# Optimization experiments

Hardware: AMD Instinct MI355X
Metric: run time of the kernel (lower is better)

Reference implementation:

```python
import jax, jax.numpy as jnp
import numpy as np

B, C, N = 8, 128, 4096
C2 = C // 2
BN_EPS = 1e-5


def setup_inputs() -> dict:
    key = jax.random.key(0)
    ks = jax.random.split(key, 8)
    s = 1.0 / np.sqrt(C)
    s2 = 1.0 / np.sqrt(C2)
    return {
        "x": jax.random.normal(ks[0], (B, C, N), dtype=jnp.float32),
        "w_qk": jax.random.uniform(ks[1], (C2, C), jnp.float32, -s, s),  # shared q/k weight
        "w_v": jax.random.uniform(ks[2], (C2, C), jnp.float32, -s, s),
        "b_v": jax.random.uniform(ks[3], (C2,), jnp.float32, -s, s),
        "w_x": jax.random.uniform(ks[4], (C2, C), jnp.float32, -s, s),
        "w_t": jax.random.uniform(ks[5], (C2, C2), jnp.float32, -s2, s2),
        "b_t": jax.random.uniform(ks[6], (C2,), jnp.float32, -s2, s2),
        "gamma": jnp.ones((C2,), jnp.float32),
        "beta": jnp.zeros((C2,), jnp.float32),
    }


def reference(x, w_qk, w_v, b_v, w_x, w_t, b_t, gamma, beta):
    # 1x1 convs are per-point linear maps: [B,C,N] -> [B,C2,N]
    x_q = jnp.einsum("oc,bcn->bno", w_qk, x)          # [B, N, C2]
    x_k = jnp.einsum("oc,bcn->bon", w_qk, x)          # [B, C2, N]
    x_v = jnp.einsum("oc,bcn->bon", w_v, x) + b_v[None, :, None]

    energy = jnp.einsum("bno,bom->bnm", x_q, x_k)     # [B, N, N]
    attn = jax.nn.softmax(energy, axis=-1)            # row softmax
    attn = attn / (1e-9 + attn.sum(axis=1, keepdims=True))  # column L1 renorm

    x_r = jnp.einsum("bon,bnm->bom", x_v, attn)       # [B, C2, N]
    x_c = jnp.einsum("oc,bcn->bon", w_x, x)           # [B, C2, N]

    d = x_c - x_r
    t = jnp.einsum("oi,bin->bon", w_t, d) + b_t[None, :, None]
    # BatchNorm1d (training-mode batch stats) over (B, N) per channel
    mean = t.mean(axis=(0, 2), keepdims=True)
    var = t.var(axis=(0, 2), keepdims=True)
    t_hat = (t - mean) * jax.lax.rsqrt(var + BN_EPS)
    x_r2 = jax.nn.relu(gamma[None, :, None] * t_hat + beta[None, :, None])
    return x_c + x_r2
```

## Files before the change

kernel.cpp:

```cpp
#include <hip/hip_runtime.h>

#define B_   8
#define C_   128
#define N_   4096
#define C2_  64

typedef __bf16 bf16x8 __attribute__((ext_vector_type(8)));
typedef float  f32x4  __attribute__((ext_vector_type(4)));

#define MFMA16(a, b, c) __builtin_amdgcn_mfma_f32_16x16x32_bf16((a), (b), (c), 0, 0, 0)

#define QK_SCALE 1.2011224087864498f

static __device__ __forceinline__ unsigned short f2bf(float f) {
    union { __bf16 b; unsigned short u; } cv;
    cv.b = (__bf16)f;
    return cv.u;
}

struct us4 { unsigned short a, b, c, d; };

static __device__ __forceinline__ void gl_lds16(const unsigned short* g, void* l) {
    __builtin_amdgcn_global_load_lds(
        (const __attribute__((address_space(1))) unsigned int*)g,
        (__attribute__((address_space(3))) unsigned int*)l,
        16, 0, 0);
}

__global__ __launch_bounds__(256) void k1_proj(
    const float* __restrict__ x, const float* __restrict__ w_qk,
    const float* __restrict__ w_v, const float* __restrict__ b_v,
    const float* __restrict__ w_x,
    unsigned short* __restrict__ qk_t, unsigned short* __restrict__ xv_bf,
    float* __restrict__ xc)
{
    __shared__ __align__(16) unsigned short w_lds[192 * 136];
    __shared__ __align__(16) unsigned short x_t[64 * 136];
    const int tid = threadIdx.x;
    const int wave = tid >> 6, lane = tid & 63;
    const int quad = lane >> 4, col = lane & 15;
    const int b = blockIdx.y;
    const int n0 = blockIdx.x * 64;

    const float* wsrc[3] = {w_qk, w_v, w_x};
    #pragma unroll
    for (int mat = 0; mat < 3; ++mat) {
        const float* wm = wsrc[mat];
        #pragma unroll
        for (int it = 0; it < 8; ++it) {
            const int idx = it * 256 + tid;
            const int o = idx >> 5, c = (idx & 31) * 4;
            const float4 v = *(const float4*)(wm + o * C_ + c);
            us4 pk;
            pk.a = f2bf(v.x); pk.b = f2bf(v.y); pk.c = f2bf(v.z); pk.d = f2bf(v.w);
            *(us4*)&w_lds[(mat * 64 + o) * 136 + c] = pk;
        }
    }
    const float* xb = x + (size_t)b * C_ * N_ + n0;
    #pragma unroll
    for (int it = 0; it < 8; ++it) {
        const int idx = it * 256 + tid;
        const int c = idx >> 4, n = (idx & 15) * 4;
        const float4 v = *(const float4*)(xb + (size_t)c * N_ + n);
        x_t[(n + 0) * 136 + c] = f2bf(v.x);
        x_t[(n + 1) * 136 + c] = f2bf(v.y);
        x_t[(n + 2) * 136 + c] = f2bf(v.z);
        x_t[(n + 3) * 136 + c] = f2bf(v.w);
    }
    __syncthreads();

    const int nw = wave * 16;
    bf16x8 bfr[4];
    #pragma unroll
    for (int kt = 0; kt < 4; ++kt)
        bfr[kt] = *(const bf16x8*)&x_t[(nw + col) * 136 + kt * 32 + quad * 8];

    const int n_g = n0 + nw + col;

    #pragma unroll
    for (int ot = 0; ot < 12; ++ot) {
        f32x4 acc = {0.f, 0.f, 0.f, 0.f};
        #pragma unroll
        for (int kt = 0; kt < 4; ++kt) {
            const bf16x8 afr = *(const bf16x8*)&w_lds[(ot * 16 + col) * 136 + kt * 32 + quad * 8];
            acc = MFMA16(afr, bfr[kt], acc);
        }
        if (ot < 4) {
            us4 pk;
            pk.a = f2bf(acc[0] * QK_SCALE); pk.b = f2bf(acc[1] * QK_SCALE);
            pk.c = f2bf(acc[2] * QK_SCALE); pk.d = f2bf(acc[3] * QK_SCALE);
            *(us4*)&qk_t[(size_t)(b * N_ + n_g) * C2_ + ot * 16 + quad * 4] = pk;
        } else if (ot < 8) {
            const float4 bv4 = *(const float4*)(b_v + (ot - 4) * 16 + quad * 4);
            const float* bvp = (const float*)&bv4;
            #pragma unroll
            for (int r = 0; r < 4; ++r)
                xv_bf[(size_t)(b * C2_ + (ot - 4) * 16 + quad * 4 + r) * N_ + n_g]
                    = f2bf(acc[r] + bvp[r]);
        } else {
            #pragma unroll
            for (int r = 0; r < 4; ++r)
                xc[(size_t)(b * C2_ + (ot - 8) * 16 + quad * 4 + r) * N_ + n_g] = acc[r];
        }
    }
}

__global__ __launch_bounds__(256) void k2_rowstats(
    const unsigned short* __restrict__ qk_t, float* __restrict__ part_rs)
{
    __shared__ __align__(16) unsigned char lds_raw[2 * 8192];
    const int tid = threadIdx.x;
    const int wave = tid >> 6, lane = tid & 63;
    const int quad = lane >> 4, col = lane & 15;
    const int b = blockIdx.x & 7;
    const int nblk = (blockIdx.x >> 3) & 31;
    const int mq = blockIdx.x >> 8;
    const int n_base = nblk * 128 + wave * 32;
    const int m_start = mq * 1024;
    const unsigned short* qb = qk_t + (size_t)b * N_ * C2_;

    bf16x8 a0[2], a1[2];
    #pragma unroll
    for (int s = 0; s < 2; ++s) {
        const unsigned short* p = qb + (size_t)(n_base + s * 16 + col) * C2_ + quad * 8;
        a0[s] = *(const bf16x8*)p;
        a1[s] = *(const bf16x8*)(p + 32);
    }

    auto stage = [&](int m0, int p) {
        unsigned char* base = lds_raw + p * 8192;
        #pragma unroll
        for (int r = 0; r < 2; ++r) {
            const int idx = r * 256 + tid;
            const int row = idx >> 3, seg = idx & 7;
            gl_lds16(qb + (size_t)(m0 + row) * C2_ + (size_t)(seg ^ (row & 7)) * 8,
                     base + idx * 16);
        }
    };

    float run_s[2][4] = {{0.f, 0.f, 0.f, 0.f}, {0.f, 0.f, 0.f, 0.f}};
    stage(m_start, 0);
    __syncthreads();

    for (int c = 0; c < 16; ++c) {
        const int p = c & 1;
        if (c + 1 < 16) stage(m_start + (c + 1) * 64, 1 - p);
        const unsigned short* qt = (const unsigned short*)(lds_raw + p * 8192);
        #pragma unroll
        for (int ms = 0; ms < 4; ++ms) {
            const int row = ms * 16 + col;
            const bf16x8 b0 = *(const bf16x8*)(qt + row * 64 + ((quad ^ (col & 7)) * 8));
            const bf16x8 b1 = *(const bf16x8*)(qt + row * 64 + (((4 + quad) ^ (col & 7)) * 8));
            #pragma unroll
            for (int s = 0; s < 2; ++s) {
                f32x4 acc = {0.f, 0.f, 0.f, 0.f};
                acc = MFMA16(a0[s], b0, acc);
                acc = MFMA16(a1[s], b1, acc);
                #pragma unroll
                for (int r = 0; r < 4; ++r)
                    run_s[s][r] += __builtin_amdgcn_exp2f(acc[r]);
            }
        }
        __syncthreads();
    }

    #pragma unroll
    for (int s = 0; s < 2; ++s)
        #pragma unroll
        for (int r = 0; r < 4; ++r) {
            #pragma unroll
            for (int off = 1; off < 16; off <<= 1)
                run_s[s][r] += __shfl_xor(run_s[s][r], off, 64);
        }
    if (col == 0) {
        #pragma unroll
        for (int s = 0; s < 2; ++s)
            #pragma unroll
            for (int r = 0; r < 4; ++r)
                part_rs[((size_t)(mq * 8 + b) << 12) + n_base + s * 16 + quad * 4 + r]
                    = run_s[s][r];
    }
}

__global__ __launch_bounds__(256) void k2b_comb(
    const float* __restrict__ part_rs, float* __restrict__ rowoff)
{
    const int i = blockIdx.x * 256 + threadIdx.x;
    const int b = i >> 12, n = i & 4095;
    float s = 0.f;
    #pragma unroll
    for (int q = 0; q < 4; ++q)
        s += part_rs[((size_t)(q * 8 + b) << 12) + n];
    rowoff[i] = __builtin_amdgcn_logf(s);
}

__global__ __launch_bounds__(256) void k3_pv(
    const unsigned short* __restrict__ qk_t, const unsigned short* __restrict__ xv_bf,
    const float* __restrict__ rowoff, float* __restrict__ yp0, float* __restrict__ yp1,
    float* __restrict__ yp2, float* __restrict__ cspart)
{
    __shared__ __align__(16) unsigned char lds_raw[32768 + 8 * 2304];
    const int tid = threadIdx.x;
    const int wave = tid >> 6, lane = tid & 63;
    const int quad = lane >> 4, col = lane & 15;
    const int b = blockIdx.x & 7;
    const int m_blk = ((blockIdx.x >> 3) & 31) * 128;
    const int sk = blockIdx.x >> 8;
    const int n_start = (sk == 0) ? 0 : 1408 + (sk - 1) * 1344;
    const int n_chunks = (sk == 0) ? 22 : 21;
    const int m_wave = m_blk + wave * 32;
    const unsigned short* qb = qk_t + (size_t)b * N_ * C2_;
    const unsigned short* vb = xv_bf + (size_t)b * C2_ * N_;
    const float* ro = rowoff + b * N_;
    float* yp = (sk == 0) ? yp0 : (sk == 1) ? yp1 : yp2;

    bf16x8 kb0[2], kb1[2];
    #pragma unroll
    for (int g = 0; g < 2; ++g) {
        const unsigned short* p = qb + (size_t)(m_wave + g * 16 + col) * C2_ + quad * 8;
        kb0[g] = *(const bf16x8*)p;
        kb1[g] = *(const bf16x8*)(p + 32);
    }

    unsigned short (*st_s[2])[72];
    st_s[0] = (unsigned short(*)[72])(lds_raw + 32768 + (wave * 2 + 0) * 2304);
    st_s[1] = (unsigned short(*)[72])(lds_raw + 32768 + (wave * 2 + 1) * 2304);

    auto stage = [&](int n0, int p) {
        unsigned char* qbase = lds_raw + p * 8192;
        unsigned char* vbase = lds_raw + 16384 + p * 8192;
        #pragma unroll
        for (int r = 0; r < 2; ++r) {
            const int idx = r * 256 + tid;
            const int row = idx >> 3, seg = idx & 7;
            const int ss = seg ^ (row & 7);
            gl_lds16(qb + (size_t)(n0 + row) * C2_ + (size_t)ss * 8, qbase + idx * 16);
            gl_lds16(vb + (size_t)row * N_ + n0 + ss * 8, vbase + idx * 16);
        }
    };

    f32x4 accY[2][4];
    #pragma unroll
    for (int g = 0; g < 2; ++g)
        #pragma unroll
        for (int os = 0; os < 4; ++os) accY[g][os] = (f32x4){0.f, 0.f, 0.f, 0.f};
    float colacc[2] = {0.f, 0.f};

    stage(n_start, 0);
    __syncthreads();

    for (int c = 0; c < n_chunks; ++c) {
        const int n0 = n_start + c * 64;
        const int p = c & 1;
        if (c + 1 < n_chunks) stage(n0 + 64, 1 - p);

        float4 ro4[4];
        #pragma unroll
        for (int ns = 0; ns < 4; ++ns)
            ro4[ns] = *(const float4*)(ro + n0 + ns * 16 + quad * 4);

        const unsigned short* qt = (const unsigned short*)(lds_raw + p * 8192);
        const unsigned short* vt = (const unsigned short*)(lds_raw + 16384 + p * 8192);

        #pragma unroll
        for (int ns = 0; ns < 4; ++ns) {
            const int row = ns * 16 + col;
            const bf16x8 qa0 = *(const bf16x8*)(qt + row * 64 + ((quad ^ (col & 7)) * 8));
            const bf16x8 qa1 = *(const bf16x8*)(qt + row * 64 + (((4 + quad) ^ (col & 7)) * 8));
            const float* rr = (const float*)&ro4[ns];
            #pragma unroll
            for (int g = 0; g < 2; ++g) {
                f32x4 acc = {0.f, 0.f, 0.f, 0.f};
                acc = MFMA16(qa0, kb0[g], acc);
                acc = MFMA16(qa1, kb1[g], acc);
                union { unsigned short us[4]; uint2 u2; } pk;
                #pragma unroll
                for (int r = 0; r < 4; ++r) {
                    const float s = __builtin_amdgcn_exp2f(acc[r] - rr[r]);
                    colacc[g] += s;
                    pk.us[r] = f2bf(s);
                }
                *(uint2*)&st_s[g][col][ns * 16 + quad * 4] = pk.u2;
            }
        }

        bf16x8 sB0[2], sB1[2];
        #pragma unroll
        for (int g = 0; g < 2; ++g) {
            sB0[g] = *(const bf16x8*)&st_s[g][col][quad * 8];
            sB1[g] = *(const bf16x8*)&st_s[g][col][32 + quad * 8];
        }
        #pragma unroll
        for (int os = 0; os < 4; ++os) {
            const int o = os * 16 + col;
            const bf16x8 va0 = *(const bf16x8*)(vt + o * 64 + ((quad ^ (col & 7)) * 8));
            const bf16x8 va1 = *(const bf16x8*)(vt + o * 64 + (((4 + quad) ^ (col & 7)) * 8));
            #pragma unroll
            for (int g = 0; g < 2; ++g) {
                accY[g][os] = MFMA16(va0, sB0[g], accY[g][os]);
                accY[g][os] = MFMA16(va1, sB1[g], accY[g][os]);
            }
        }
        __syncthreads();
    }

    #pragma unroll
    for (int g = 0; g < 2; ++g) {
        colacc[g] += __shfl_xor(colacc[g], 16, 64);
        colacc[g] += __shfl_xor(colacc[g], 32, 64);
        if (lane < 16)
            cspart[((size_t)sk * 8 + b) * N_ + m_wave + g * 16 + col] = colacc[g];
        #pragma unroll
        for (int os = 0; os < 4; ++os)
            #pragma unroll
            for (int r = 0; r < 4; ++r)
                yp[(size_t)(b * C2_ + os * 16 + quad * 4 + r) * N_ + m_wave + g * 16 + col]
                    = accY[g][os][r];
    }
}

__global__ __launch_bounds__(256) void k3b_comb(
    float* yp0, const float* __restrict__ yp1, const float* __restrict__ yp2,
    const float* __restrict__ cspart)
{
    const int idx4 = blockIdx.x * 256 + threadIdx.x;
    const int b = idx4 >> 16;
    const int m4 = idx4 & 1023;
    const float4 y0 = ((const float4*)yp0)[idx4];
    const float4 y1 = ((const float4*)yp1)[idx4];
    const float4 y2 = ((const float4*)yp2)[idx4];
    const float4 c0 = ((const float4*)cspart)[b * 1024 + m4];
    const float4 c1 = ((const float4*)cspart)[8192 + b * 1024 + m4];
    const float4 c2 = ((const float4*)cspart)[16384 + b * 1024 + m4];
    float4 r;
    r.x = (y0.x + y1.x + y2.x) / (1e-9f + c0.x + c1.x + c2.x);
    r.y = (y0.y + y1.y + y2.y) / (1e-9f + c0.y + c1.y + c2.y);
    r.z = (y0.z + y1.z + y2.z) / (1e-9f + c0.z + c1.z + c2.z);
    r.w = (y0.w + y1.w + y2.w) / (1e-9f + c0.w + c1.w + c2.w);
    ((float4*)yp0)[idx4] = r;
}

__global__ __launch_bounds__(256) void k4_t(
    const float* __restrict__ xc, const float* __restrict__ xr,
    const float* __restrict__ w_t, const float* __restrict__ b_t,
    float* __restrict__ t_buf)
{
    __shared__ float d_lds[64][64];
    __shared__ float w_lds[64][64];
    const int b = blockIdx.y;
    const int n0 = blockIdx.x * 64;
    const size_t base = (size_t)b * C2_ * N_;

    for (int idx = threadIdx.x; idx < 4096; idx += 256) {
        const int i = idx >> 6, n = idx & 63;
        const size_t g = base + (size_t)i * N_ + n0 + n;
        d_lds[i][n] = xc[g] - xr[g];
        w_lds[i][n] = w_t[idx];
    }
    __syncthreads();

    const int n = threadIdx.x & 63, ow = (threadIdx.x >> 6) * 16;
    float acc[16];
    #pragma unroll
    for (int oo = 0; oo < 16; ++oo) acc[oo] = 0.f;
    for (int i = 0; i < 64; ++i) {
        const float dv = d_lds[i][n];
        #pragma unroll
        for (int oo = 0; oo < 16; ++oo)
            acc[oo] += w_lds[ow + oo][i] * dv;
    }
    #pragma unroll
    for (int oo = 0; oo < 16; ++oo)
        t_buf[base + (size_t)(ow + oo) * N_ + n0 + n] = acc[oo] + b_t[ow + oo];
}

__global__ __launch_bounds__(256) void k5_bnstats(
    const float* __restrict__ t_buf, float* __restrict__ bn)
{
    const int o = blockIdx.x;
    float s = 0.f, s2 = 0.f;
    for (int b = 0; b < B_; ++b) {
        const float4* p = (const float4*)(t_buf + (size_t)(b * C2_ + o) * N_);
        for (int j = threadIdx.x; j < N_ / 4; j += 256) {
            const float4 v = p[j];
            s  += v.x + v.y + v.z + v.w;
            s2 += v.x * v.x + v.y * v.y + v.z * v.z + v.w * v.w;
        }
    }
    #pragma unroll
    for (int off = 1; off < 64; off <<= 1) {
        s  += __shfl_xor(s, off, 64);
        s2 += __shfl_xor(s2, off, 64);
    }
    __shared__ float red[2][4];
    if ((threadIdx.x & 63) == 0) {
        red[0][threadIdx.x >> 6] = s;
        red[1][threadIdx.x >> 6] = s2;
    }
    __syncthreads();
    if (threadIdx.x == 0) {
        bn[o]       = red[0][0] + red[0][1] + red[0][2] + red[0][3];
        bn[64 + o]  = red[1][0] + red[1][1] + red[1][2] + red[1][3];
    }
}

__global__ __launch_bounds__(256) void k6_out(
    const float* __restrict__ xc, const float* __restrict__ t_buf,
    const float* __restrict__ bn, const float* __restrict__ gamma,
    const float* __restrict__ beta, float* __restrict__ out)
{
    const int idx = blockIdx.x * 256 + threadIdx.x;
    const int o = (idx >> 10) & 63;
    const float invC = 1.0f / (float)(B_ * N_);
    const float mean = bn[o] * invC;
    const float var  = bn[64 + o] * invC - mean * mean;
    const float sc = gamma[o] * rsqrtf(var + 1e-5f);
    const float sh = beta[o] - mean * sc;
    const float4 t4 = ((const float4*)t_buf)[idx];
    const float4 c4 = ((const float4*)xc)[idx];
    float4 r;
    r.x = c4.x + fmaxf(0.f, sc * t4.x + sh);
    r.y = c4.y + fmaxf(0.f, sc * t4.y + sh);
    r.z = c4.z + fmaxf(0.f, sc * t4.z + sh);
    r.w = c4.w + fmaxf(0.f, sc * t4.w + sh);
    ((float4*)out)[idx] = r;
}

extern "C" void kernel_launch(void* const* d_in, const int* in_sizes, int n_in,
                              void* d_out, int out_size, void* d_ws, size_t ws_size,
                              hipStream_t stream) {
    const float* x     = (const float*)d_in[0];
    const float* w_qk  = (const float*)d_in[1];
    const float* w_v   = (const float*)d_in[2];
    const float* b_v   = (const float*)d_in[3];
    const float* w_x   = (const float*)d_in[4];
    const float* w_t   = (const float*)d_in[5];
    const float* b_t   = (const float*)d_in[6];
    const float* gamma = (const float*)d_in[7];
    const float* beta  = (const float*)d_in[8];
    float* out = (float*)d_out;

    char* ws = (char*)d_ws;
    unsigned short* qk_t  = (unsigned short*)ws;
    unsigned short* xv_bf = (unsigned short*)(ws + (4  << 20));
    float* xc      = (float*)(ws + (8  << 20));
    float* xr_yp0  = (float*)(ws + (16 << 20));
    float* tb_yp1  = (float*)(ws + (24 << 20));
    float* part_rs = (float*)(ws + (32 << 20));
    float* rowoff  = (float*)(ws + (32 << 20) + (512 << 10));
    float* cspart  = (float*)(ws + (32 << 20) + (640 << 10));
    float* bn      = (float*)(ws + (33 << 20));
    float* yp2     = out;

    hipLaunchKernelGGL(k1_proj,     dim3(64, 8),  256, 0, stream,
                       x, w_qk, w_v, b_v, w_x, qk_t, xv_bf, xc);
    hipLaunchKernelGGL(k2_rowstats, dim3(1024),   256, 0, stream, qk_t, part_rs);
    hipLaunchKernelGGL(k2b_comb,    dim3(128),    256, 0, stream, part_rs, rowoff);
    hipLaunchKernelGGL(k3_pv,       dim3(768),    256, 0, stream,
                       qk_t, xv_bf, rowoff, xr_yp0, tb_yp1, yp2, cspart);
    hipLaunchKernelGGL(k3b_comb,    dim3(2048),   256, 0, stream, xr_yp0, tb_yp1, yp2, cspart);
    hipLaunchKernelGGL(k4_t,        dim3(64, 8),  256, 0, stream, xc, xr_yp0, w_t, b_t, tb_yp1);
    hipLaunchKernelGGL(k5_bnstats,  dim3(64),     256, 0, stream, tb_yp1, bn);
    hipLaunchKernelGGL(k6_out,      dim3(2048),   256, 0, stream, xc, tb_yp1, bn, gamma, beta, out);
}
```

Measured before the change: 197.0 us.

## Fold softmax row normalization into V and column sums via MFMA

Instead of subtracting a per-row log offset before exp in the PV kernel, the row reciprocal sums are computed once and multiplied into the value tensor by a new scaling kernel. The column sums come from an extra MFMA against a bf16 weight vector rather than scalar accumulation. The PV kernel retiles so each wave covers 64 columns and half of the n-chunk, and combines the two halves through LDS at the end. Row-stats work is also repartitioned into larger n tiles. The aim is to remove the subtraction and scalar adds in the inner loop, at the cost of an extra pass over V, more bf16 rounding, and higher register pressure.

```diff
diff --git a/kernel.cpp b/kernel.cpp
--- a/kernel.cpp
+++ b/kernel.cpp
@@ -16,6 +16,11 @@
     union { __bf16 b; unsigned short u; } cv;
     cv.b = (__bf16)f;
     return cv.u;
+}
+static __device__ __forceinline__ float bf2f(unsigned short u) {
+    union { unsigned int u; float f; } cv;
+    cv.u = ((unsigned int)u) << 16;
+    return cv.f;
 }
 
 struct us4 { unsigned short a, b, c, d; };
@@ -113,15 +118,15 @@
     const int wave = tid >> 6, lane = tid & 63;
     const int quad = lane >> 4, col = lane & 15;
     const int b = blockIdx.x & 7;
-    const int nblk = (blockIdx.x >> 3) & 31;
-    const int mq = blockIdx.x >> 8;
-    const int n_base = nblk * 128 + wave * 32;
-    const int m_start = mq * 1024;
+    const int nblk = (blockIdx.x >> 3) & 15;
+    const int mq = blockIdx.x >> 7;
+    const int n_base = nblk * 256 + wave * 64;
+    const int m_start = mq * 512;
     const unsigned short* qb = qk_t + (size_t)b * N_ * C2_;
 
-    bf16x8 a0[2], a1[2];
-    #pragma unroll
-    for (int s = 0; s < 2; ++s) {
+    bf16x8 a0[4], a1[4];
+    #pragma unroll
+    for (int s = 0; s < 4; ++s) {
         const unsigned short* p = qb + (size_t)(n_base + s * 16 + col) * C2_ + quad * 8;
         a0[s] = *(const bf16x8*)p;
         a1[s] = *(const bf16x8*)(p + 32);
@@ -138,13 +143,18 @@
         }
     };
 
-    float run_s[2][4] = {{0.f, 0.f, 0.f, 0.f}, {0.f, 0.f, 0.f, 0.f}};
+    float run_s[4][4];
+    #pragma unroll
+    for (int s = 0; s < 4; ++s)
+        #pragma unroll
+        for (int r = 0; r < 4; ++r) run_s[s][r] = 0.f;
+
     stage(m_start, 0);
     __syncthreads();
 
-    for (int c = 0; c < 16; ++c) {
+    for (int c = 0; c < 8; ++c) {
         const int p = c & 1;
-        if (c + 1 < 16) stage(m_start + (c + 1) * 64, 1 - p);
+        if (c + 1 < 8) stage(m_start + (c + 1) * 64, 1 - p);
         const unsigned short* qt = (const unsigned short*)(lds_raw + p * 8192);
         #pragma unroll
         for (int ms = 0; ms < 4; ++ms) {
@@ -152,7 +162,7 @@
             const bf16x8 b0 = *(const bf16x8*)(qt + row * 64 + ((quad ^ (col & 7)) * 8));
             const bf16x8 b1 = *(const bf16x8*)(qt + row * 64 + (((4 + quad) ^ (col & 7)) * 8));
             #pragma unroll
-            for (int s = 0; s < 2; ++s) {
+            for (int s = 0; s < 4; ++s) {
                 f32x4 acc = {0.f, 0.f, 0.f, 0.f};
                 acc = MFMA16(a0[s], b0, acc);
                 acc = MFMA16(a1[s], b1, acc);
@@ -165,7 +175,7 @@
     }
 
     #pragma unroll
-    for (int s = 0; s < 2; ++s)
+    for (int s = 0; s < 4; ++s)
         #pragma unroll
         for (int r = 0; r < 4; ++r) {
             #pragma unroll
@@ -174,7 +184,7 @@
         }
     if (col == 0) {
         #pragma unroll
-        for (int s = 0; s < 2; ++s)
+        for (int s = 0; s < 4; ++s)
             #pragma unroll
             for (int r = 0; r < 4; ++r)
                 part_rs[((size_t)(mq * 8 + b) << 12) + n_base + s * 16 + quad * 4 + r]
@@ -183,48 +193,67 @@
 }
 
 __global__ __launch_bounds__(256) void k2b_comb(
-    const float* __restrict__ part_rs, float* __restrict__ rowoff)
+    const float* __restrict__ part_rs, float* __restrict__ winv,
+    unsigned short* __restrict__ wbf)
 {
     const int i = blockIdx.x * 256 + threadIdx.x;
     const int b = i >> 12, n = i & 4095;
     float s = 0.f;
     #pragma unroll
-    for (int q = 0; q < 4; ++q)
+    for (int q = 0; q < 8; ++q)
         s += part_rs[((size_t)(q * 8 + b) << 12) + n];
-    rowoff[i] = __builtin_amdgcn_logf(s);
-}
-
-__global__ __launch_bounds__(256) void k3_pv(
+    const float w = 1.0f / s;
+    winv[i] = w;
+    wbf[i] = f2bf(w);
+}
+
+__global__ __launch_bounds__(256) void k2c_scale(
+    unsigned short* __restrict__ xv_bf, const float* __restrict__ winv)
+{
+    const int t = blockIdx.x * 256 + threadIdx.x;
+    const int flat = t * 4;
+    const int b = flat >> 18;
+    const int n = flat & 4095;
+    const float4 w4 = *(const float4*)(winv + b * 4096 + n);
+    us4 v = *(us4*)(xv_bf + flat);
+    v.a = f2bf(bf2f(v.a) * w4.x);
+    v.b = f2bf(bf2f(v.b) * w4.y);
+    v.c = f2bf(bf2f(v.c) * w4.z);
+    v.d = f2bf(bf2f(v.d) * w4.w);
+    *(us4*)(xv_bf + flat) = v;
+}
+
+__global__ __launch_bounds__(256, 3) void k3_pv(
     const unsigned short* __restrict__ qk_t, const unsigned short* __restrict__ xv_bf,
-    const float* __restrict__ rowoff, float* __restrict__ yp0, float* __restrict__ yp1,
-    float* __restrict__ yp2, float* __restrict__ cspart)
-{
-    __shared__ __align__(16) unsigned char lds_raw[32768 + 8 * 2304];
+    const unsigned short* __restrict__ wbf,
+    float* __restrict__ yp0, float* __restrict__ yp1, float* __restrict__ yp2,
+    float* __restrict__ cspart)
+{
+    __shared__ __align__(16) unsigned char lds_raw[32768 + 4 * 5120];
     const int tid = threadIdx.x;
     const int wave = tid >> 6, lane = tid & 63;
     const int quad = lane >> 4, col = lane & 15;
+    const int nh2 = wave & 1, mh = wave >> 1;
     const int b = blockIdx.x & 7;
     const int m_blk = ((blockIdx.x >> 3) & 31) * 128;
     const int sk = blockIdx.x >> 8;
     const int n_start = (sk == 0) ? 0 : 1408 + (sk - 1) * 1344;
     const int n_chunks = (sk == 0) ? 22 : 21;
-    const int m_wave = m_blk + wave * 32;
+    const int m_wave = m_blk + mh * 64;
     const unsigned short* qb = qk_t + (size_t)b * N_ * C2_;
     const unsigned short* vb = xv_bf + (size_t)b * C2_ * N_;
-    const float* ro = rowoff + b * N_;
+    const unsigned short* wb = wbf + b * N_;
     float* yp = (sk == 0) ? yp0 : (sk == 1) ? yp1 : yp2;
 
-    bf16x8 kb0[2], kb1[2];
-    #pragma unroll
-    for (int g = 0; g < 2; ++g) {
+    bf16x8 kb0[4], kb1[4];
+    #pragma unroll
+    for (int g = 0; g < 4; ++g) {
         const unsigned short* p = qb + (size_t)(m_wave + g * 16 + col) * C2_ + quad * 8;
         kb0[g] = *(const bf16x8*)p;
         kb1[g] = *(const bf16x8*)(p + 32);
     }
 
-    unsigned short (*st_s[2])[72];
-    st_s[0] = (unsigned short(*)[72])(lds_raw + 32768 + (wave * 2 + 0) * 2304);
-    st_s[1] = (unsigned short(*)[72])(lds_raw + 32768 + (wave * 2 + 1) * 2304);
+    unsigned short* stS = (unsigned short*)(lds_raw + 32768 + wave * 5120);
 
     auto stage = [&](int n0, int p) {
         unsigned char* qbase = lds_raw + p * 8192;
@@ -239,12 +268,14 @@
         }
     };
 
-    f32x4 accY[2][4];
-    #pragma unroll
-    for (int g = 0; g < 2; ++g)
+    f32x4 accY[4][4];
+    #pragma unroll
+    for (int g = 0; g < 4; ++g)
         #pragma unroll
         for (int os = 0; os < 4; ++os) accY[g][os] = (f32x4){0.f, 0.f, 0.f, 0.f};
-    float colacc[2] = {0.f, 0.f};
+    f32x4 csacc[4];
+    #pragma unroll
+    for (int g = 0; g < 4; ++g) csacc[g] = (f32x4){0.f, 0.f, 0.f, 0.f};
 
     stage(n_start, 0);
     __syncthreads();
@@ -254,68 +285,78 @@
         const int p = c & 1;
         if (c + 1 < n_chunks) stage(n0 + 64, 1 - p);
 
-        float4 ro4[4];
-        #pragma unroll
-        for (int ns = 0; ns < 4; ++ns)
-            ro4[ns] = *(const float4*)(ro + n0 + ns * 16 + quad * 4);
-
         const unsigned short* qt = (const unsigned short*)(lds_raw + p * 8192);
         const unsigned short* vt = (const unsigned short*)(lds_raw + 16384 + p * 8192);
 
-        #pragma unroll
-        for (int ns = 0; ns < 4; ++ns) {
-            const int row = ns * 16 + col;
+        const bf16x8 wfrag = *(const bf16x8*)(wb + n0 + nh2 * 32 + quad * 8);
+
+        #pragma unroll
+        for (int ns = 0; ns < 2; ++ns) {
+            const int row = nh2 * 32 + ns * 16 + col;
             const bf16x8 qa0 = *(const bf16x8*)(qt + row * 64 + ((quad ^ (col & 7)) * 8));
             const bf16x8 qa1 = *(const bf16x8*)(qt + row * 64 + (((4 + quad) ^ (col & 7)) * 8));
-            const float* rr = (const float*)&ro4[ns];
-            #pragma unroll
-            for (int g = 0; g < 2; ++g) {
+            #pragma unroll
+            for (int g = 0; g < 4; ++g) {
                 f32x4 acc = {0.f, 0.f, 0.f, 0.f};
                 acc = MFMA16(qa0, kb0[g], acc);
                 acc = MFMA16(qa1, kb1[g], acc);
                 union { unsigned short us[4]; uint2 u2; } pk;
                 #pragma unroll
+                for (int r = 0; r < 4; ++r)
+                    pk.us[r] = f2bf(__builtin_amdgcn_exp2f(acc[r]));
+                *(uint2*)&stS[(g * 16 + col) * 40 + ns * 16 + quad * 4] = pk.u2;
+            }
+        }
+
+        bf16x8 sB[4];
+        #pragma unroll
+        for (int g = 0; g < 4; ++g)
+            sB[g] = *(const bf16x8*)&stS[(g * 16 + col) * 40 + quad * 8];
+
+        #pragma unroll
+        for (int g = 0; g < 4; ++g)
+            csacc[g] = MFMA16(wfrag, sB[g], csacc[g]);
+
+        #pragma unroll
+        for (int os = 0; os < 4; ++os) {
+            const bf16x8 va = *(const bf16x8*)(vt + (os * 16 + col) * 64 +
+                                               (((nh2 * 4 + quad) ^ (col & 7)) * 8));
+            #pragma unroll
+            for (int g = 0; g < 4; ++g)
+                accY[g][os] = MFMA16(va, sB[g], accY[g][os]);
+        }
+        __syncthreads();
+    }
+
+    float* cmb = (float*)lds_raw;
+    float* csc = (float*)(lds_raw + 32768);
+    if (nh2 == 1) {
+        #pragma unroll
+        for (int g = 0; g < 4; ++g) {
+            #pragma unroll
+            for (int os = 0; os < 4; ++os)
+                #pragma unroll
+                for (int r = 0; r < 4; ++r)
+                    cmb[((mh * 16 + g * 4 + os) * 4 + r) * 64 + lane] = accY[g][os][r];
+            csc[(mh * 4 + g) * 64 + lane] = csacc[g][0];
+        }
+    }
+    __syncthreads();
+    if (nh2 == 0) {
+        #pragma unroll
+        for (int g = 0; g < 4; ++g) {
+            const float cs = csacc[g][0] + csc[(mh * 4 + g) * 64 + lane];
+            if (lane < 16)
+                cspart[((size_t)sk * 8 + b) * N_ + m_wave + g * 16 + lane] = cs;
+            #pragma unroll
+            for (int os = 0; os < 4; ++os)
+                #pragma unroll
                 for (int r = 0; r < 4; ++r) {
-                    const float s = __builtin_amdgcn_exp2f(acc[r] - rr[r]);
-                    colacc[g] += s;
-                    pk.us[r] = f2bf(s);
+                    const float v = accY[g][os][r] +
+                        cmb[((mh * 16 + g * 4 + os) * 4 + r) * 64 + lane];
+                    yp[(size_t)(b * C2_ + os * 16 + quad * 4 + r) * N_ + m_wave + g * 16 + col] = v;
                 }
-                *(uint2*)&st_s[g][col][ns * 16 + quad * 4] = pk.u2;
-            }
-        }
-
-        bf16x8 sB0[2], sB1[2];
-        #pragma unroll
-        for (int g = 0; g < 2; ++g) {
-            sB0[g] = *(const bf16x8*)&st_s[g][col][quad * 8];
-            sB1[g] = *(const bf16x8*)&st_s[g][col][32 + quad * 8];
-        }
-        #pragma unroll
-        for (int os = 0; os < 4; ++os) {
-            const int o = os * 16 + col;
-            const bf16x8 va0 = *(const bf16x8*)(vt + o * 64 + ((quad ^ (col & 7)) * 8));
-            const bf16x8 va1 = *(const bf16x8*)(vt + o * 64 + (((4 + quad) ^ (col & 7)) * 8));
-            #pragma unroll
-            for (int g = 0; g < 2; ++g) {
-                accY[g][os] = MFMA16(va0, sB0[g], accY[g][os]);
-                accY[g][os] = MFMA16(va1, sB1[g], accY[g][os]);
-            }
-        }
-        __syncthreads();
-    }
-
-    #pragma unroll
-    for (int g = 0; g < 2; ++g) {
-        colacc[g] += __shfl_xor(colacc[g], 16, 64);
-        colacc[g] += __shfl_xor(colacc[g], 32, 64);
-        if (lane < 16)
-            cspart[((size_t)sk * 8 + b) * N_ + m_wave + g * 16 + col] = colacc[g];
-        #pragma unroll
-        for (int os = 0; os < 4; ++os)
-            #pragma unroll
-            for (int r = 0; r < 4; ++r)
-                yp[(size_t)(b * C2_ + os * 16 + quad * 4 + r) * N_ + m_wave + g * 16 + col]
-                    = accY[g][os][r];
+        }
     }
 }
 
@@ -447,17 +488,19 @@
     float* xr_yp0  = (float*)(ws + (16 << 20));
     float* tb_yp1  = (float*)(ws + (24 << 20));
     float* part_rs = (float*)(ws + (32 << 20));
-    float* rowoff  = (float*)(ws + (32 << 20) + (512 << 10));
-    float* cspart  = (float*)(ws + (32 << 20) + (640 << 10));
-    float* bn      = (float*)(ws + (33 << 20));
+    float* cspart  = (float*)(ws + (32 << 20));
+    float* winv    = (float*)(ws + (33 << 20));
+    unsigned short* wbf = (unsigned short*)(ws + (33 << 20) + (128 << 10));
+    float* bn      = (float*)(ws + (33 << 20) + (192 << 10));
     float* yp2     = out;
 
     hipLaunchKernelGGL(k1_proj,     dim3(64, 8),  256, 0, stream,
                        x, w_qk, w_v, b_v, w_x, qk_t, xv_bf, xc);
     hipLaunchKernelGGL(k2_rowstats, dim3(1024),   256, 0, stream, qk_t, part_rs);
-    hipLaunchKernelGGL(k2b_comb,    dim3(128),    256, 0, stream, part_rs, rowoff);
+    hipLaunchKernelGGL(k2b_comb,    dim3(128),    256, 0, stream, part_rs, winv, wbf);
+    hipLaunchKernelGGL(k2c_scale,   dim3(2048),   256, 0, stream, xv_bf, winv);
     hipLaunchKernelGGL(k3_pv,       dim3(768),    256, 0, stream,
-                       qk_t, xv_bf, rowoff, xr_yp0, tb_yp1, yp2, cspart);
+                       qk_t, xv_bf, wbf, xr_yp0, tb_yp1, yp2, cspart);
     hipLaunchKernelGGL(k3b_comb,    dim3(2048),   256, 0, stream, xr_yp0, tb_yp1, yp2, cspart);
     hipLaunchKernelGGL(k4_t,        dim3(64, 8),  256, 0, stream, xc, xr_yp0, w_t, b_t, tb_yp1);
     hipLaunchKernelGGL(k5_bnstats,  dim3(64),     256, 0, stream, tb_yp1, bn);
```

New measurement: 192.7 us. 2.2% less time.
